# Optimization experiments

Hardware: AMD Instinct MI355X
Metric: run time of the kernel (lower is better)

The kernel has to match this reference:

```python
import jax, jax.numpy as jnp
import numpy as np
import math

B, N, DEG, D, L = 256, 256, 8, 128, 3  # graphs, nodes/graph, avg degree, feature dim, pool layers


def setup_inputs() -> dict:
    key = jax.random.key(0)
    ks = jax.random.split(key, 12)
    Nn = B * N
    E = B * N * DEG
    x = jax.random.normal(ks[0], (Nn, D), jnp.float32)
    # edges strictly within each graph; graphs laid out contiguously (graph b owns nodes [b*N, (b+1)*N))
    offs = jnp.repeat(jnp.arange(B, dtype=jnp.int32) * N, N * DEG)
    src = offs + jax.random.randint(ks[1], (E,), 0, N, dtype=jnp.int32)
    dst = offs + jax.random.randint(ks[2], (E,), 0, N, dtype=jnp.int32)
    edge_index = jnp.stack([src, dst])
    graph_indices = jnp.repeat(jnp.arange(B, dtype=jnp.int32), N)
    s = 1.0 / math.sqrt(D)
    def w(k, shape):
        return jax.random.normal(k, shape, jnp.float32) * s
    return {
        "x": x,
        "edge_index": edge_index,
        "graph_indices": graph_indices,
        "num_graphs": B,
        "Wq": w(ks[3], (L, D, D)), "bq": jnp.zeros((L, D), jnp.float32),
        "Wk": w(ks[4], (L, D, D)), "bk": jnp.zeros((L, D), jnp.float32),
        "Wv": w(ks[5], (L, D, D)), "bv": jnp.zeros((L, D), jnp.float32),
        "Wskip": w(ks[6], (L, D, D)), "bskip": jnp.zeros((L, D), jnp.float32),
        "Wt": w(ks[7], (L, D, D)), "bt": jnp.zeros((L, D), jnp.float32),
        "gamma": jnp.ones((L, D), jnp.float32) + 0.1 * jax.random.normal(ks[8], (L, D), jnp.float32),
        "beta": 0.1 * jax.random.normal(ks[9], (L, D), jnp.float32),
        "pool_w": w(ks[10], (L, D)),
    }


def reference(x, edge_index, graph_indices, num_graphs, Wq, bq, Wk, bk, Wv, bv,
              Wskip, bskip, Wt, bt, gamma, beta, pool_w):
    Bg = int(num_graphs)
    Nn, d = x.shape
    n = Nn // Bg                       # nodes per graph (equal-size graphs)
    src, dst = edge_index[0], edge_index[1]
    mask = jnp.ones(src.shape, bool)   # edge validity mask (shapes stay static across layers)
    NEG = jnp.float32(-1e30)
    inv_sqrt_d = 1.0 / jnp.sqrt(jnp.float32(d))
    feats = []
    for i in range(Wq.shape[0]):
        Nn_cur = x.shape[0]
        # --- TransformerConv (heads=1, concat, root_weight=True, no edge_dim, eval: no dropout) ---
        q = x @ Wq[i] + bq[i]
        k = x @ Wk[i] + bk[i]
        v = x @ Wv[i] + bv[i]
        logits = jnp.einsum('ed,ed->e', q[dst], k[src]) * inv_sqrt_d   # [E]
        logits = jnp.where(mask, logits, NEG)
        m = jax.ops.segment_max(logits, dst, num_segments=Nn_cur)
        m = jnp.where(m > NEG / 2, m, 0.0)                             # guard empty segments
        ex = jnp.where(mask, jnp.exp(logits - m[dst]), 0.0)
        denom = jax.ops.segment_sum(ex, dst, num_segments=Nn_cur)
        alpha = ex / jnp.maximum(denom[dst], 1e-16)                    # scatter-softmax over incoming edges
        agg = jax.ops.segment_sum(alpha[:, None] * v[src], dst, num_segments=Nn_cur)
        x = agg + (x @ Wskip[i] + bskip[i])
        # --- Linear + ReLU ---
        x = jax.nn.relu(x @ Wt[i] + bt[i])
        # --- BatchNorm1d (training-mode batch stats, eps=1e-5) ---
        mu = x.mean(0)
        var = x.var(0)
        x = (x - mu) / jnp.sqrt(var + 1e-5) * gamma[i] + beta[i]
        # --- TopKPooling(ratio=0.5, nonlinearity=tanh) ---
        w_ = pool_w[i]
        score = jnp.tanh((x @ w_) / jnp.linalg.norm(w_))               # [Nn_cur]
        kk = n // 2
        _, idx = jax.lax.top_k(score.reshape(Bg, n), kk)               # [B, kk] per-graph top-k
        perm = (jnp.arange(Bg, dtype=idx.dtype)[:, None] * n + idx).reshape(-1)
        x = x[perm] * score[perm][:, None]
        # re-index edges; drop edges touching removed nodes via mask
        newid = jnp.full((Nn_cur,), -1, dtype=src.dtype).at[perm].set(
            jnp.arange(Bg * kk, dtype=src.dtype))
        s2, d2 = newid[src], newid[dst]
        mask = mask & (s2 >= 0) & (d2 >= 0)
        src = jnp.where(mask, s2, 0)
        dst = jnp.where(mask, d2, 0)
        n = kk
        # --- readout: gmp | gap | gsp per graph ---
        xr = x.reshape(Bg, n, d)
        feats.append(jnp.concatenate([xr.max(1), xr.mean(1), xr.sum(1)], axis=-1))
    return jnp.concatenate(feats, axis=-1)   # [B, L*3*d]
```

## Files before the change

### kernel.cpp

```cpp
#include <hip/hip_runtime.h>
#include <hip/hip_bf16.h>
#include <math.h>

#define DD     128
#define NGRAPH 256
#define ECAPG  2048
#define ETOT   (NGRAPH*ECAPG)
#define NMAX   65536

typedef __attribute__((ext_vector_type(8))) short bf16x8;
typedef __attribute__((ext_vector_type(4))) float f32x4;

__device__ inline unsigned short rne_bf16(float x){
  union { float f; unsigned u; } c; c.f = x;
  unsigned u = c.u;
  return (unsigned short)((u + 0x7FFFu + ((u>>16)&1u)) >> 16);
}
__device__ inline float bf16f(unsigned short h){
  union { unsigned u; float f; } c; c.u = ((unsigned)h)<<16; return c.f;
}

__device__ inline void gload_lds16(const void* g, void* l){
  __builtin_amdgcn_global_load_lds(
      (const __attribute__((address_space(1))) unsigned*)g,
      (__attribute__((address_space(3))) unsigned*)l, 16, 0, 0);
}

__global__ __launch_bounds__(128) void k_wnorm(const float* pw, float* wni){
  int l = blockIdx.x, t = threadIdx.x;
  __shared__ float s[128];
  float v = pw[l*DD + t];
  s[t] = v*v; __syncthreads();
  for (int o=64;o>0;o>>=1){ if (t<o) s[t]+=s[t+o]; __syncthreads(); }
  if (t==0) wni[l] = 1.0f/sqrtf(s[0]);
}

__global__ __launch_bounds__(128) void k_wprep(const float* Wq, const float* Wk, const float* Wv,
                                               const float* Ws, const float* Wt,
                                               unsigned short* whi, unsigned short* wlo){
  int b = blockIdx.x;
  int w = b>>7, krow = b&127, n = threadIdx.x;
  int layer = w/5, which = w - layer*5;
  const float* W = (which==0)?Wq:(which==1)?Wk:(which==2)?Wv:(which==3)?Ws:Wt;
  float v = W[(size_t)layer*DD*DD + krow*DD + n];
  unsigned short h = rne_bf16(v);
  unsigned short l = rne_bf16(v - bf16f(h));
  whi[(size_t)w*DD*DD + (size_t)n*DD + krow] = h;
  wlo[(size_t)w*DD*DD + (size_t)n*DD + krow] = l;
}

__global__ __launch_bounds__(256) void k_xsplit(const float* __restrict__ X,
                                                unsigned short* __restrict__ xh,
                                                unsigned short* __restrict__ xl, int total4){
  int i = blockIdx.x*256 + threadIdx.x;
  if (i >= total4) return;
  float4 v = ((const float4*)X)[i];
  unsigned short h0=rne_bf16(v.x), h1=rne_bf16(v.y), h2=rne_bf16(v.z), h3=rne_bf16(v.w);
  unsigned short l0=rne_bf16(v.x-bf16f(h0)), l1=rne_bf16(v.y-bf16f(h1)),
                 l2=rne_bf16(v.z-bf16f(h2)), l3=rne_bf16(v.w-bf16f(h3));
  uint2 uh, ul;
  uh.x = (unsigned)h0 | ((unsigned)h1<<16); uh.y = (unsigned)h2 | ((unsigned)h3<<16);
  ul.x = (unsigned)l0 | ((unsigned)l1<<16); ul.y = (unsigned)l2 | ((unsigned)l3<<16);
  ((uint2*)xh)[i] = uh; ((uint2*)xl)[i] = ul;
}

__global__ __launch_bounds__(256) void k_csr(const int* __restrict__ src, const int* __restrict__ dst,
                                             int n, int* row_start, int* row_end, int* ssrc){
  int g = blockIdx.x, t = threadIdx.x;
  const int E = ECAPG;
  int base = g*ECAPG;
  __shared__ int lsrc[ECAPG];
  __shared__ unsigned char ldst8[ECAPG];
  __shared__ unsigned char slotc[ECAPG];
  __shared__ unsigned short off[64][256];
  __shared__ int sc[256];
  __shared__ int rstart[256];
  for (int i=t; i<64*256/2; i+=256) ((unsigned*)off)[i] = 0;
  for (int i=t; i<E; i+=256){ lsrc[i]=src[base+i]; ldst8[i]=(unsigned char)(dst[base+i]-g*n); }
  __syncthreads();
  if (t < 64){
    int e0=t*32;
    for (int i=e0;i<e0+32;i++){ int d=ldst8[i]; slotc[i]=(unsigned char)off[t][d]; off[t][d]++; }
  }
  __syncthreads();
  int tot=0;
  if (t<n){
    for (int c=0;c<64;c++){ int tmp=off[c][t]; off[c][t]=(unsigned short)tot; tot+=tmp; }
  }
  sc[t] = (t<n)?tot:0;
  __syncthreads();
  for (int o=1;o<256;o<<=1){ int add=(t>=o)?sc[t-o]:0; __syncthreads(); sc[t]+=add; __syncthreads(); }
  if (t<n){
    int rs = sc[t]-tot;
    rstart[t]=rs;
    row_start[g*n+t]=base+rs; row_end[g*n+t]=base+rs+tot;
  }
  __syncthreads();
  if (t<64){
    int e0=t*32;
    for (int i=e0;i<e0+32;i++){
      int d=ldst8[i];
      ssrc[base + rstart[d] + off[t][d] + slotc[i]] = lsrc[i];
    }
  }
}

struct GArgs {
  const unsigned short* whi[4];
  const unsigned short* wlo[4];
  const float* bias[4];
  float*       O[4];
};

template<int BN>
__global__ __launch_bounds__(256) void k_gemm_mfma(const unsigned short* __restrict__ XHg,
                                                   const unsigned short* __restrict__ XLg,
                                                   GArgs a, float* __restrict__ psum,
                                                   float* __restrict__ psq){
  __shared__ unsigned short XH[128][32], XL[128][32], WHs[128][32], WLs[128][32];
  int head = BN ? 0 : blockIdx.y;
  const unsigned short* WH = a.whi[head];
  const unsigned short* WL = a.wlo[head];
  size_t rowBase = (size_t)blockIdx.x*128;
  int t = threadIdx.x;
  int w = t>>6, l = t&63;
  int wr = (w>>1)*64, wc = (w&1)*64;
  int lr = l&15, lk = (l>>4)*8;
  f32x4 acc[4][4] = {};
  char* bXH = (char*)&XH[0][0];
  char* bXL = (char*)&XL[0][0];
  char* bWH = (char*)&WHs[0][0];
  char* bWL = (char*)&WLs[0][0];
  for (int kc=0; kc<128; kc+=32){
    __syncthreads();
    #pragma unroll
    for (int s2=0; s2<2; s2++){
      int j  = (w*2+s2)*64 + l;
      int r  = j>>2, g = j&3;
      int gc = (g ^ ((r>>1)&3))*8;
      size_t segOff = (size_t)(w*2+s2)*1024;
      size_t gx = (rowBase + r)*DD + kc + gc;
      size_t gw = (size_t)r*DD + kc + gc;
      gload_lds16(XHg + gx, bXH + segOff);
      gload_lds16(XLg + gx, bXL + segOff);
      gload_lds16(WH  + gw, bWH + segOff);
      gload_lds16(WL  + gw, bWL + segOff);
    }
    __syncthreads();
    bf16x8 ah[4], al[4], bh[4], bl[4];
    #pragma unroll
    for (int m=0;m<4;m++){
      int rr = wr + m*16 + lr;
      int bo = rr*64 + ((lk*2) ^ (((rr>>1)&3)<<4));
      ah[m] = *(const bf16x8*)(bXH + bo);
      al[m] = *(const bf16x8*)(bXL + bo);
    }
    #pragma unroll
    for (int n=0;n<4;n++){
      int rr = wc + n*16 + lr;
      int bo = rr*64 + ((lk*2) ^ (((rr>>1)&3)<<4));
      bh[n] = *(const bf16x8*)(bWH + bo);
      bl[n] = *(const bf16x8*)(bWL + bo);
    }
    #pragma unroll
    for (int m=0;m<4;m++){
      #pragma unroll
      for (int n=0;n<4;n++){
        acc[m][n] = __builtin_amdgcn_mfma_f32_16x16x32_bf16(ah[m], bh[n], acc[m][n], 0,0,0);
        acc[m][n] = __builtin_amdgcn_mfma_f32_16x16x32_bf16(ah[m], bl[n], acc[m][n], 0,0,0);
        acc[m][n] = __builtin_amdgcn_mfma_f32_16x16x32_bf16(al[m], bh[n], acc[m][n], 0,0,0);
      }
    }
  }
  float* O = a.O[head];
  const float* bias = a.bias[head];
  float cs[4] = {0.f,0.f,0.f,0.f}, cq[4] = {0.f,0.f,0.f,0.f};
  #pragma unroll
  for (int n=0;n<4;n++){
    int col = wc + n*16 + lr;
    float bv = bias[col];
    #pragma unroll
    for (int m=0;m<4;m++){
      int rb = wr + m*16 + (l>>4)*4;
      #pragma unroll
      for (int r=0;r<4;r++){
        float o = acc[m][n][r] + bv;
        if (BN) o = fmaxf(o, 0.f);
        O[(rowBase + rb + r)*DD + col] = o;
        if (BN){ cs[n] += o; cq[n] += o*o; }
      }
    }
  }
  if (BN){
    __syncthreads();
    float* redS = (float*)&XH[0][0];
    float* redQ = (float*)&XL[0][0];
    int rg = w*4 + (l>>4);
    #pragma unroll
    for (int n=0;n<4;n++){
      int col = wc + n*16 + lr;
      redS[rg*128 + col] = cs[n];
      redQ[rg*128 + col] = cq[n];
    }
    __syncthreads();
    if (t < 128){
      int c = t, w0 = (c>=64) ? 1 : 0;
      float s = 0.f, s2 = 0.f;
      #pragma unroll
      for (int dw=0; dw<2; dw++){
        int ww = w0 + dw*2;
        #pragma unroll
        for (int lq=0; lq<4; lq++){
          s  += redS[(ww*4+lq)*128 + c];
          s2 += redQ[(ww*4+lq)*128 + c];
        }
      }
      psum[blockIdx.x*DD + c] = s;
      psq [blockIdx.x*DD + c] = s2;
    }
  }
}

__global__ __launch_bounds__(256) void k_attn_par(
    const float* __restrict__ q, const float* __restrict__ k, const float* __restrict__ v,
    const int* __restrict__ row_start, const int* __restrict__ row_end,
    const int* __restrict__ ssrc, const float* __restrict__ skip,
    unsigned short* __restrict__ xh, unsigned short* __restrict__ xl)
{
  __shared__ float lg[4][2][128];
  __shared__ int   se[4][2][128];
  int nb8 = gridDim.x >> 3;
  int p = blockIdx.x;
  int lb = (p&7)*nb8 + (p>>3);
  int w = threadIdx.x>>6, l = threadIdx.x&63;
  int h = l>>5, q32 = l&31;
  int node = lb*8 + w*2 + h;
  int s0 = row_start[node];
  int deg = row_end[node]-s0; if (deg>128) deg=128;
  int maxd = max(deg, __shfl_xor(deg, 32, 64));
  int grp = q32>>3, gl = q32&7;
  const float isd = 0.088388347648318447f;
  unsigned qoff = ((unsigned)node<<7) + (unsigned)(gl<<4);
  float4 qv0 = *(const float4*)(q + qoff);
  float4 qv1 = *(const float4*)(q + qoff + 4);
  float4 qv2 = *(const float4*)(q + qoff + 8);
  float4 qv3 = *(const float4*)(q + qoff + 12);
  if (q32==0) se[w][h][0] = 0;
  for (int base=0; base<maxd; base+=4){
    int e = base + grp;
    int eok = (e<deg);
    int s = ssrc[s0 + (eok ? e : 0)];
    unsigned ko = ((unsigned)s<<7) + (unsigned)(gl<<4);
    const float* kp = k + ko;
    float4 k0=*(const float4*)kp, k1=*(const float4*)(kp+4),
           k2=*(const float4*)(kp+8), k3=*(const float4*)(kp+12);
    float pd = qv0.x*k0.x+qv0.y*k0.y+qv0.z*k0.z+qv0.w*k0.w
             + qv1.x*k1.x+qv1.y*k1.y+qv1.z*k1.z+qv1.w*k1.w
             + qv2.x*k2.x+qv2.y*k2.y+qv2.z*k2.z+qv2.w*k2.w
             + qv3.x*k3.x+qv3.y*k3.y+qv3.z*k3.z+qv3.w*k3.w;
    pd += __shfl_xor(pd,1,64); pd += __shfl_xor(pd,2,64); pd += __shfl_xor(pd,4,64);
    if (gl==0 && eok){ lg[w][h][e] = pd*isd; se[w][h][e] = s; }
  }
  float x0v = (q32    <deg) ? lg[w][h][q32]    : -1e30f;
  float x1v = (32+q32 <deg) ? lg[w][h][32+q32] : -1e30f;
  float x2v = (64+q32 <deg) ? lg[w][h][64+q32] : -1e30f;
  float x3v = (96+q32 <deg) ? lg[w][h][96+q32] : -1e30f;
  float m = fmaxf(fmaxf(x0v,x1v), fmaxf(x2v,x3v));
  #pragma unroll
  for (int o=16;o>0;o>>=1) m = fmaxf(m, __shfl_xor(m,o,64));
  float e0 = (q32   <deg) ? __expf(x0v-m) : 0.f;
  float e1 = (32+q32<deg) ? __expf(x1v-m) : 0.f;
  float e2 = (64+q32<deg) ? __expf(x2v-m) : 0.f;
  float e3 = (96+q32<deg) ? __expf(x3v-m) : 0.f;
  float dn = (e0+e1)+(e2+e3);
  #pragma unroll
  for (int o=16;o>0;o>>=1) dn += __shfl_xor(dn,o,64);
  float rd = 1.0f/fmaxf(dn, 1e-16f);
  if (q32   <deg) lg[w][h][q32]    = e0*rd;
  if (32+q32<deg) lg[w][h][32+q32] = e1*rd;
  if (64+q32<deg) lg[w][h][64+q32] = e2*rd;
  if (96+q32<deg) lg[w][h][96+q32] = e3*rd;
  float4 a = make_float4(0.f,0.f,0.f,0.f);
  unsigned dcol = (unsigned)(q32<<2);
  for (int e=0; e<maxd; e++){
    int eok = (e<deg);
    int s  = se[w][h][eok ? e : 0];
    float al = eok ? lg[w][h][e] : 0.f;
    float4 vv = *(const float4*)(v + (((unsigned)s<<7) + dcol));
    a.x += al*vv.x; a.y += al*vv.y; a.z += al*vv.z; a.w += al*vv.w;
  }
  unsigned ob = ((unsigned)node<<7) + dcol;
  float4 sk = *(const float4*)(skip + ob);
  float x0 = sk.x + a.x, x1 = sk.y + a.y, x2 = sk.z + a.z, x3 = sk.w + a.w;
  unsigned short h0=rne_bf16(x0), h1=rne_bf16(x1), h2=rne_bf16(x2), h3=rne_bf16(x3);
  unsigned short lo0=rne_bf16(x0-bf16f(h0)), lo1=rne_bf16(x1-bf16f(h1)),
                 lo2=rne_bf16(x2-bf16f(h2)), lo3=rne_bf16(x3-bf16f(h3));
  uint2 uh, ul;
  uh.x = (unsigned)h0 | ((unsigned)h1<<16); uh.y = (unsigned)h2 | ((unsigned)h3<<16);
  ul.x = (unsigned)lo0 | ((unsigned)lo1<<16); ul.y = (unsigned)lo2 | ((unsigned)lo3<<16);
  *(uint2*)(xh + ob) = uh;
  *(uint2*)(xl + ob) = ul;
}

__global__ __launch_bounds__(256) void k_bnfin(const float* __restrict__ psum,
                                               const float* __restrict__ psq,
                                               float* mu, float* istd, float invN, int nblk){
  int c = blockIdx.x, t = threadIdx.x;
  __shared__ float sh[256], sh2[256];
  float s=0.f, s2=0.f;
  for (int b=t; b<nblk; b+=256){ s += psum[b*DD+c]; s2 += psq[b*DD+c]; }
  sh[t]=s; sh2[t]=s2; __syncthreads();
  for (int o=128;o>0;o>>=1){
    if (t<o){ sh[t]+=sh[t+o]; sh2[t]+=sh2[t+o]; }
    __syncthreads();
  }
  if (t==0){
    float m = sh[0]*invN;
    float var = fmaxf(sh2[0]*invN - m*m, 0.f);
    mu[c]=m; istd[c] = 1.0f/sqrtf(var + 1e-5f);
  }
}

__global__ __launch_bounds__(256) void k_pool(
    const float* __restrict__ h, const float* __restrict__ mu, const float* __restrict__ istd,
    const float* __restrict__ gma, const float* __restrict__ bta,
    const float* __restrict__ pw, const float* __restrict__ wni, int layer, int n,
    const int* __restrict__ osrc, const int* __restrict__ odst, const int* __restrict__ oecnt,
    unsigned short* __restrict__ xh, unsigned short* __restrict__ xl,
    float* __restrict__ out,
    int* __restrict__ nsrc, int* __restrict__ ndst, int* __restrict__ necnt,
    int* __restrict__ row_start, int* __restrict__ row_end, int* __restrict__ ssrc, int do_edges)
{
  int g = blockIdx.x, t = threadIdx.x;
  int kk = n>>1;
  __shared__ float bnp[5][128];
  __shared__ float ss[256];
  __shared__ int   sel[128];
  __shared__ float skp[128];
  __shared__ int   nid[256];
  __shared__ float redm[4][128], rdsum[4][128];
  __shared__ int   esrc[ECAPG], edst[ECAPG];
  __shared__ int   sc[256];
  __shared__ unsigned short off2[64][128];
  __shared__ unsigned char  slot2[ECAPG];
  __shared__ int   rstart2[128];

  if (t<128){ bnp[0][t]=mu[t]; bnp[1][t]=istd[t]; bnp[2][t]=gma[t]; bnp[3][t]=bta[t]; bnp[4][t]=pw[t]; }
  __syncthreads();
  if (t<n){
    const float* hr = h + ((size_t)g*n + t)*DD;
    float dot = 0.f;
    for (int c=0;c<DD;c+=4){
      float4 hv = *(const float4*)(hr+c);
      dot += ((hv.x-bnp[0][c+0])*bnp[1][c+0]*bnp[2][c+0]+bnp[3][c+0])*bnp[4][c+0];
      dot += ((hv.y-bnp[0][c+1])*bnp[1][c+1]*bnp[2][c+1]+bnp[3][c+1])*bnp[4][c+1];
      dot += ((hv.z-bnp[0][c+2])*bnp[1][c+2]*bnp[2][c+2]+bnp[3][c+2])*bnp[4][c+2];
      dot += ((hv.w-bnp[0][c+3])*bnp[1][c+3]*bnp[2][c+3]+bnp[3][c+3])*bnp[4][c+3];
    }
    ss[t] = tanhf(dot * wni[0]);
  }
  __syncthreads();
  if (t<n){
    float si = ss[t]; int rank = 0;
    for (int j=0;j<n;j++){ float sj = ss[j]; rank += (sj>si)||((sj==si)&&(j<t)); }
    if (rank<kk){ sel[rank]=t; skp[rank]=si; nid[t]=rank; } else nid[t]=-1;
  }
  __syncthreads();
  int w = t>>6, l = t&63, d0 = l*2;
  float m0=-1e30f, m1=-1e30f, sm0=0.f, sm1=0.f;
  for (int p=w; p<kk; p+=4){
    int srow = sel[p]; float scv = skp[p];
    float2 hv = *(const float2*)(h + ((size_t)g*n + srow)*DD + d0);
    float x0 = ((hv.x-bnp[0][d0  ])*bnp[1][d0  ]*bnp[2][d0  ]+bnp[3][d0  ])*scv;
    float x1 = ((hv.y-bnp[0][d0+1])*bnp[1][d0+1]*bnp[2][d0+1]+bnp[3][d0+1])*scv;
    m0 = fmaxf(m0,x0); m1 = fmaxf(m1,x1); sm0 += x0; sm1 += x1;
    unsigned short h0=rne_bf16(x0), h1=rne_bf16(x1);
    unsigned short l0=rne_bf16(x0-bf16f(h0)), l1=rne_bf16(x1-bf16f(h1));
    size_t ob = ((size_t)g*kk + p)*DD + d0;
    *(unsigned*)(xh+ob) = (unsigned)h0 | ((unsigned)h1<<16);
    *(unsigned*)(xl+ob) = (unsigned)l0 | ((unsigned)l1<<16);
  }
  redm[w][d0]=m0; redm[w][d0+1]=m1; rdsum[w][d0]=sm0; rdsum[w][d0+1]=sm1;
  __syncthreads();
  if (t<128){
    float mx = fmaxf(fmaxf(redm[0][t],redm[1][t]), fmaxf(redm[2][t],redm[3][t]));
    float sm = rdsum[0][t]+rdsum[1][t]+rdsum[2][t]+rdsum[3][t];
    float* ob = out + (size_t)g*1152 + layer*384;
    ob[t]=mx; ob[128+t]=sm/(float)kk; ob[256+t]=sm;
  }
  if (!do_edges) return;
  int E = oecnt ? oecnt[g] : ECAPG;
  int base = g*ECAPG;
  int cl = 0;
  for (int j=0;j<8;j++){ int i=t*8+j;
    if (i<E){ int ns=nid[osrc[base+i]-g*n], nd=nid[odst[base+i]-g*n]; if ((ns|nd)>=0) cl++; } }
  sc[t]=cl; __syncthreads();
  for (int o=1;o<256;o<<=1){ int add=(t>=o)?sc[t-o]:0; __syncthreads(); sc[t]+=add; __syncthreads(); }
  int off = sc[t]-cl;
  for (int j=0;j<8;j++){ int i=t*8+j;
    if (i<E){ int ns=nid[osrc[base+i]-g*n], nd=nid[odst[base+i]-g*n];
      if ((ns|nd)>=0){ esrc[off]=ns; edst[off]=nd; off++; } } }
  int Etot = sc[255];
  __syncthreads();
  if (t==0) necnt[g]=Etot;
  for (int i=t;i<Etot;i+=256){ nsrc[base+i]=esrc[i]+g*kk; ndst[base+i]=edst[i]+g*kk; }
  for (int i=t; i<64*128/2; i+=256) ((unsigned*)off2)[i] = 0;
  __syncthreads();
  int nch = (Etot+31)>>5;
  if (t<nch){
    int e0=t*32, e1 = (e0+32<Etot)?(e0+32):Etot;
    for (int i=e0;i<e1;i++){ int d=edst[i]; slot2[i]=(unsigned char)off2[t][d]; off2[t][d]++; }
  }
  __syncthreads();
  int tot=0;
  if (t<kk){
    for (int c=0;c<nch;c++){ int tmp=off2[c][t]; off2[c][t]=(unsigned short)tot; tot+=tmp; }
  }
  sc[t] = (t<kk)?tot:0;
  __syncthreads();
  for (int o=1;o<256;o<<=1){ int add=(t>=o)?sc[t-o]:0; __syncthreads(); sc[t]+=add; __syncthreads(); }
  if (t<kk){
    int rs = sc[t]-tot;
    rstart2[t]=rs;
    row_start[g*kk+t]=base+rs; row_end[g*kk+t]=base+rs+tot;
  }
  __syncthreads();
  if (t<nch){
    int e0=t*32, e1 = (e0+32<Etot)?(e0+32):Etot;
    for (int i=e0;i<e1;i++){
      int d=edst[i];
      ssrc[base + rstart2[d] + off2[t][d] + slot2[i]] = esrc[i] + g*kk;
    }
  }
}

extern "C" void kernel_launch(void* const* d_in, const int* in_sizes, int n_in,
                              void* d_out, int out_size, void* d_ws, size_t ws_size,
                              hipStream_t stream){
  const float* x0   = (const float*)d_in[0];
  const int*   eidx = (const int*)d_in[1];
  const float* Wq = (const float*)d_in[4];  const float* bq = (const float*)d_in[5];
  const float* Wk = (const float*)d_in[6];  const float* bk = (const float*)d_in[7];
  const float* Wv = (const float*)d_in[8];  const float* bv = (const float*)d_in[9];
  const float* Wsk= (const float*)d_in[10]; const float* bsk= (const float*)d_in[11];
  const float* Wt = (const float*)d_in[12]; const float* bt = (const float*)d_in[13];
  const float* gamma = (const float*)d_in[14]; const float* beta = (const float*)d_in[15];
  const float* pw = (const float*)d_in[16];

  char* w8 = (char*)d_ws;
  size_t off = 0;
  auto alloc = [&](size_t bytes)->void*{ void* p = w8+off; off += (bytes+255)&~(size_t)255; return p; };

  float* qb  = (float*)alloc((size_t)NMAX*DD*4);
  float* kb  = (float*)alloc((size_t)NMAX*DD*4);
  float* vb  = (float*)alloc((size_t)NMAX*DD*4);
  float* xsb = (float*)alloc((size_t)NMAX*DD*4);
  unsigned short* xh = (unsigned short*)alloc((size_t)NMAX*DD*2);
  unsigned short* xl = (unsigned short*)alloc((size_t)NMAX*DD*2);
  unsigned short* whi = (unsigned short*)alloc((size_t)15*DD*DD*2);
  unsigned short* wlo = (unsigned short*)alloc((size_t)15*DD*DD*2);
  float* psum = (float*)alloc((size_t)512*DD*4);
  float* psq  = (float*)alloc((size_t)512*DD*4);
  float* mu   = (float*)alloc(DD*4);
  float* istd = (float*)alloc(DD*4);
  float* wni  = (float*)alloc(64);
  int* row_start = (int*)alloc(NMAX*4);
  int* row_end   = (int*)alloc(NMAX*4);
  int* ssrc      = (int*)alloc(ETOT*4);
  int* srcA = (int*)alloc(ETOT*4);
  int* dstA = (int*)alloc(ETOT*4);
  int* srcB = (int*)alloc(ETOT*4);
  int* dstB = (int*)alloc(ETOT*4);
  int* ecntA = (int*)alloc(NGRAPH*4);
  int* ecntB = (int*)alloc(NGRAPH*4);

  k_wnorm<<<3,128,0,stream>>>(pw, wni);
  k_wprep<<<15*128,128,0,stream>>>(Wq, Wk, Wv, Wsk, Wt, whi, wlo);
  k_xsplit<<<NMAX/8,256,0,stream>>>(x0, xh, xl, NMAX*32);
  k_csr<<<NGRAPH,256,0,stream>>>(eidx, eidx+ETOT, 256, row_start, row_end, ssrc);

  const int* csrc = eidx;
  const int* cdst = eidx + ETOT;
  const int* cecnt = nullptr;
  int n = 256;

  for (int layer=0; layer<3; layer++){
    int Nn = NGRAPH * n;
    int kk = n/2;

    GArgs h4;
    h4.whi[0]=whi+(size_t)(layer*5+0)*DD*DD; h4.wlo[0]=wlo+(size_t)(layer*5+0)*DD*DD; h4.bias[0]=bq +layer*DD; h4.O[0]=qb;
    h4.whi[1]=whi+(size_t)(layer*5+1)*DD*DD; h4.wlo[1]=wlo+(size_t)(layer*5+1)*DD*DD; h4.bias[1]=bk +layer*DD; h4.O[1]=kb;
    h4.whi[2]=whi+(size_t)(layer*5+2)*DD*DD; h4.wlo[2]=wlo+(size_t)(layer*5+2)*DD*DD; h4.bias[2]=bv +layer*DD; h4.O[2]=vb;
    h4.whi[3]=whi+(size_t)(layer*5+3)*DD*DD; h4.wlo[3]=wlo+(size_t)(layer*5+3)*DD*DD; h4.bias[3]=bsk+layer*DD; h4.O[3]=xsb;
    k_gemm_mfma<0><<<dim3(Nn/128,4),256,0,stream>>>(xh, xl, h4, nullptr, nullptr);

    k_attn_par<<<Nn/8,256,0,stream>>>(qb, kb, vb, row_start, row_end, ssrc, xsb, xh, xl);

    GArgs h1;
    h1.whi[0]=whi+(size_t)(layer*5+4)*DD*DD; h1.wlo[0]=wlo+(size_t)(layer*5+4)*DD*DD; h1.bias[0]=bt+layer*DD; h1.O[0]=qb;
    h1.whi[1]=h1.whi[0]; h1.wlo[1]=h1.wlo[0]; h1.bias[1]=h1.bias[0]; h1.O[1]=qb;
    h1.whi[2]=h1.whi[0]; h1.wlo[2]=h1.wlo[0]; h1.bias[2]=h1.bias[0]; h1.O[2]=qb;
    h1.whi[3]=h1.whi[0]; h1.wlo[3]=h1.wlo[0]; h1.bias[3]=h1.bias[0]; h1.O[3]=qb;
    k_gemm_mfma<1><<<dim3(Nn/128,1),256,0,stream>>>(xh, xl, h1, psum, psq);

    k_bnfin<<<128,256,0,stream>>>(psum, psq, mu, istd, 1.0f/(float)Nn, Nn/128);

    int* nsrc  = (layer==0) ? srcA : srcB;
    int* ndst  = (layer==0) ? dstA : dstB;
    int* necnt = (layer==0) ? ecntA : ecntB;
    k_pool<<<NGRAPH,256,0,stream>>>(qb, mu, istd, gamma+layer*DD, beta+layer*DD,
                                    pw+layer*DD, wni+layer, layer, n,
                                    csrc, cdst, cecnt, xh, xl, (float*)d_out,
                                    nsrc, ndst, necnt, row_start, row_end, ssrc, layer<2 ? 1 : 0);

    csrc = nsrc; cdst = ndst; cecnt = necnt;
    n = kk;
  }
}
```

Baseline: 322.6 us.

## Fuse four projection GEMMs into one kernel with full X tile in LDS

The GEMM kernel now loads the whole 128x128 hi/lo bf16 X tile into LDS once per block and loops over all heads (Q, K, V, skip) inside the block, instead of launching a separate block per head that reloads X. Weight fragments are read straight from global memory (relying on L2/L1 caching) rather than staged through LDS. This cuts redundant X traffic and the per-k-chunk LDS staging barriers. In exchange it uses 64KB of LDS per block, which lowers occupancy, launches 4x fewer blocks for the QKV step, and issues uncoalesced global weight loads with no latency hiding.

```diff
diff --git a/kernel.cpp b/kernel.cpp
--- a/kernel.cpp
+++ b/kernel.cpp
@@ -112,111 +112,105 @@
   float*       O[4];
 };
 
-template<int BN>
-__global__ __launch_bounds__(256) void k_gemm_mfma(const unsigned short* __restrict__ XHg,
-                                                   const unsigned short* __restrict__ XLg,
-                                                   GArgs a, float* __restrict__ psum,
-                                                   float* __restrict__ psq){
-  __shared__ unsigned short XH[128][32], XL[128][32], WHs[128][32], WLs[128][32];
-  int head = BN ? 0 : blockIdx.y;
-  const unsigned short* WH = a.whi[head];
-  const unsigned short* WL = a.wlo[head];
+template<int NH, int BN>
+__global__ __launch_bounds__(256) void k_gemm_fused(const unsigned short* __restrict__ XHg,
+                                                    const unsigned short* __restrict__ XLg,
+                                                    GArgs a, float* __restrict__ psum,
+                                                    float* __restrict__ psq){
+  __shared__ unsigned short XH[128*128], XL[128*128];
   size_t rowBase = (size_t)blockIdx.x*128;
   int t = threadIdx.x;
   int w = t>>6, l = t&63;
   int wr = (w>>1)*64, wc = (w&1)*64;
-  int lr = l&15, lk = (l>>4)*8;
-  f32x4 acc[4][4] = {};
-  char* bXH = (char*)&XH[0][0];
-  char* bXL = (char*)&XL[0][0];
-  char* bWH = (char*)&WHs[0][0];
-  char* bWL = (char*)&WLs[0][0];
-  for (int kc=0; kc<128; kc+=32){
-    __syncthreads();
-    #pragma unroll
-    for (int s2=0; s2<2; s2++){
-      int j  = (w*2+s2)*64 + l;
-      int r  = j>>2, g = j&3;
-      int gc = (g ^ ((r>>1)&3))*8;
-      size_t segOff = (size_t)(w*2+s2)*1024;
-      size_t gx = (rowBase + r)*DD + kc + gc;
-      size_t gw = (size_t)r*DD + kc + gc;
-      gload_lds16(XHg + gx, bXH + segOff);
-      gload_lds16(XLg + gx, bXL + segOff);
-      gload_lds16(WH  + gw, bWH + segOff);
-      gload_lds16(WL  + gw, bWL + segOff);
-    }
-    __syncthreads();
-    bf16x8 ah[4], al[4], bh[4], bl[4];
-    #pragma unroll
-    for (int m=0;m<4;m++){
-      int rr = wr + m*16 + lr;
-      int bo = rr*64 + ((lk*2) ^ (((rr>>1)&3)<<4));
-      ah[m] = *(const bf16x8*)(bXH + bo);
-      al[m] = *(const bf16x8*)(bXL + bo);
-    }
-    #pragma unroll
-    for (int n=0;n<4;n++){
-      int rr = wc + n*16 + lr;
-      int bo = rr*64 + ((lk*2) ^ (((rr>>1)&3)<<4));
-      bh[n] = *(const bf16x8*)(bWH + bo);
-      bl[n] = *(const bf16x8*)(bWL + bo);
-    }
-    #pragma unroll
-    for (int m=0;m<4;m++){
+  int lr = l&15, lkg = l>>4;
+  #pragma unroll
+  for (int s=0; s<8; s++){
+    int jb = (s*4 + w)*64;
+    int j  = jb + l;
+    int r = j>>4, c16 = j&15;
+    int sc = (c16 ^ (r&7))*8;
+    size_t gx = (rowBase + r)*DD + sc;
+    gload_lds16(XHg + gx, (char*)XH + (size_t)jb*16);
+    gload_lds16(XLg + gx, (char*)XL + (size_t)jb*16);
+  }
+  __syncthreads();
+  for (int head=0; head<NH; head++){
+    const unsigned short* __restrict__ WH = a.whi[head];
+    const unsigned short* __restrict__ WL = a.wlo[head];
+    f32x4 acc[4][4] = {};
+    for (int kc=0; kc<4; kc++){
+      bf16x8 ah[4], al[4], bh[4], bl[4];
+      int kg = kc*4 + lkg;
+      int lk = kc*32 + lkg*8;
+      #pragma unroll
+      for (int m=0;m<4;m++){
+        int rr = wr + m*16 + lr;
+        int eo = rr*128 + ((kg ^ (rr&7))<<3);
+        ah[m] = *(const bf16x8*)(XH + eo);
+        al[m] = *(const bf16x8*)(XL + eo);
+      }
       #pragma unroll
       for (int n=0;n<4;n++){
-        acc[m][n] = __builtin_amdgcn_mfma_f32_16x16x32_bf16(ah[m], bh[n], acc[m][n], 0,0,0);
-        acc[m][n] = __builtin_amdgcn_mfma_f32_16x16x32_bf16(ah[m], bl[n], acc[m][n], 0,0,0);
-        acc[m][n] = __builtin_amdgcn_mfma_f32_16x16x32_bf16(al[m], bh[n], acc[m][n], 0,0,0);
+        int cc = wc + n*16 + lr;
+        bh[n] = *(const bf16x8*)(WH + (size_t)cc*DD + lk);
+        bl[n] = *(const bf16x8*)(WL + (size_t)cc*DD + lk);
+      }
+      #pragma unroll
+      for (int m=0;m<4;m++){
+        #pragma unroll
+        for (int n=0;n<4;n++){
+          acc[m][n] = __builtin_amdgcn_mfma_f32_16x16x32_bf16(ah[m], bh[n], acc[m][n], 0,0,0);
+          acc[m][n] = __builtin_amdgcn_mfma_f32_16x16x32_bf16(ah[m], bl[n], acc[m][n], 0,0,0);
+          acc[m][n] = __builtin_amdgcn_mfma_f32_16x16x32_bf16(al[m], bh[n], acc[m][n], 0,0,0);
+        }
       }
     }
-  }
-  float* O = a.O[head];
-  const float* bias = a.bias[head];
-  float cs[4] = {0.f,0.f,0.f,0.f}, cq[4] = {0.f,0.f,0.f,0.f};
-  #pragma unroll
-  for (int n=0;n<4;n++){
-    int col = wc + n*16 + lr;
-    float bv = bias[col];
-    #pragma unroll
-    for (int m=0;m<4;m++){
-      int rb = wr + m*16 + (l>>4)*4;
-      #pragma unroll
-      for (int r=0;r<4;r++){
-        float o = acc[m][n][r] + bv;
-        if (BN) o = fmaxf(o, 0.f);
-        O[(rowBase + rb + r)*DD + col] = o;
-        if (BN){ cs[n] += o; cq[n] += o*o; }
-      }
-    }
-  }
-  if (BN){
-    __syncthreads();
-    float* redS = (float*)&XH[0][0];
-    float* redQ = (float*)&XL[0][0];
-    int rg = w*4 + (l>>4);
+    float* O = a.O[head];
+    const float* bias = a.bias[head];
+    float cs[4] = {0.f,0.f,0.f,0.f}, cq[4] = {0.f,0.f,0.f,0.f};
     #pragma unroll
     for (int n=0;n<4;n++){
       int col = wc + n*16 + lr;
-      redS[rg*128 + col] = cs[n];
-      redQ[rg*128 + col] = cq[n];
-    }
-    __syncthreads();
-    if (t < 128){
-      int c = t, w0 = (c>=64) ? 1 : 0;
-      float s = 0.f, s2 = 0.f;
+      float bv = bias[col];
       #pragma unroll
-      for (int dw=0; dw<2; dw++){
-        int ww = w0 + dw*2;
+      for (int m=0;m<4;m++){
+        int rb = wr + m*16 + (l>>4)*4;
         #pragma unroll
-        for (int lq=0; lq<4; lq++){
-          s  += redS[(ww*4+lq)*128 + c];
-          s2 += redQ[(ww*4+lq)*128 + c];
+        for (int r=0;r<4;r++){
+          float o = acc[m][n][r] + bv;
+          if (BN) o = fmaxf(o, 0.f);
+          O[(rowBase + rb + r)*DD + col] = o;
+          if (BN){ cs[n] += o; cq[n] += o*o; }
         }
       }
-      psum[blockIdx.x*DD + c] = s;
-      psq [blockIdx.x*DD + c] = s2;
+    }
+    if (BN){
+      __syncthreads();
+      float* redS = (float*)XH;
+      float* redQ = (float*)XL;
+      int rg = w*4 + (l>>4);
+      #pragma unroll
+      for (int n=0;n<4;n++){
+        int col = wc + n*16 + lr;
+        redS[rg*128 + col] = cs[n];
+        redQ[rg*128 + col] = cq[n];
+      }
+      __syncthreads();
+      if (t < 128){
+        int c = t, w0 = (c>=64) ? 1 : 0;
+        float s = 0.f, s2 = 0.f;
+        #pragma unroll
+        for (int dw=0; dw<2; dw++){
+          int ww = w0 + dw*2;
+          #pragma unroll
+          for (int lq=0; lq<4; lq++){
+            s  += redS[(ww*4+lq)*128 + c];
+            s2 += redQ[(ww*4+lq)*128 + c];
+          }
+        }
+        psum[blockIdx.x*DD + c] = s;
+        psq [blockIdx.x*DD + c] = s2;
+      }
     }
   }
 }
@@ -493,7 +487,7 @@
     h4.whi[1]=whi+(size_t)(layer*5+1)*DD*DD; h4.wlo[1]=wlo+(size_t)(layer*5+1)*DD*DD; h4.bias[1]=bk +layer*DD; h4.O[1]=kb;
     h4.whi[2]=whi+(size_t)(layer*5+2)*DD*DD; h4.wlo[2]=wlo+(size_t)(layer*5+2)*DD*DD; h4.bias[2]=bv +layer*DD; h4.O[2]=vb;
     h4.whi[3]=whi+(size_t)(layer*5+3)*DD*DD; h4.wlo[3]=wlo+(size_t)(layer*5+3)*DD*DD; h4.bias[3]=bsk+layer*DD; h4.O[3]=xsb;
-    k_gemm_mfma<0><<<dim3(Nn/128,4),256,0,stream>>>(xh, xl, h4, nullptr, nullptr);
+    k_gemm_fused<4,0><<<Nn/128,256,0,stream>>>(xh, xl, h4, nullptr, nullptr);
 
     k_attn_par<<<Nn/8,256,0,stream>>>(qb, kb, vb, row_start, row_end, ssrc, xsb, xh, xl);
 
@@ -502,7 +496,7 @@
     h1.whi[1]=h1.whi[0]; h1.wlo[1]=h1.wlo[0]; h1.bias[1]=h1.bias[0]; h1.O[1]=qb;
     h1.whi[2]=h1.whi[0]; h1.wlo[2]=h1.wlo[0]; h1.bias[2]=h1.bias[0]; h1.O[2]=qb;
     h1.whi[3]=h1.whi[0]; h1.wlo[3]=h1.wlo[0]; h1.bias[3]=h1.bias[0]; h1.O[3]=qb;
-    k_gemm_mfma<1><<<dim3(Nn/128,1),256,0,stream>>>(xh, xl, h1, psum, psq);
+    k_gemm_fused<1,1><<<Nn/128,256,0,stream>>>(xh, xl, h1, psum, psq);
 
     k_bnfin<<<128,256,0,stream>>>(psum, psq, mu, istd, 1.0f/(float)Nn, Nn/128);
 
```

Result: slower. 339.5 us (+5.2%).
